# Kernel optimization log

Measured on AMD Instinct MI355X. Metric: run time of the kernel, lower is better.

The kernel has to match this reference:

```python
import jax, jax.numpy as jnp
import numpy as np

IN_DIM, HID, HEADS, LAYERS = 15, 128, 8, 6
N_NODES, N_EDGES = 20000, 160000
HC = HEADS * HID  # 1024
LN_EPS = 1e-5


def setup_inputs() -> dict:
    key = jax.random.key(0)
    ks = jax.random.split(key, 12)
    w = lambda k, shape: (jax.random.normal(k, shape, jnp.float32) * 0.02)
    return {
        "x": jax.random.normal(ks[0], (N_NODES, IN_DIM), jnp.float32),
        "edge_index": jax.random.randint(ks[1], (2, N_EDGES), 0, N_NODES, jnp.int32),
        # input projection
        "Win": w(ks[2], (IN_DIM, HID)), "b_in": jnp.zeros((HID,), jnp.float32),
        # per-layer TransformerConv params (stacked over LAYERS)
        "Wq": w(ks[3], (LAYERS, HID, HC)), "bq": jnp.zeros((LAYERS, HC), jnp.float32),
        "Wk": w(ks[4], (LAYERS, HID, HC)), "bk": jnp.zeros((LAYERS, HC), jnp.float32),
        "Wv": w(ks[5], (LAYERS, HID, HC)), "bv": jnp.zeros((LAYERS, HC), jnp.float32),
        "Wskip": w(ks[6], (LAYERS, HID, HC)), "bskip": jnp.zeros((LAYERS, HC), jnp.float32),
        "Wbeta": w(ks[7], (LAYERS, 3 * HC, 1)),  # lin_beta, bias=False
        # LayerNorm(hid*heads) and output proj per layer
        "ln_g": jnp.ones((LAYERS, HC), jnp.float32), "ln_b": jnp.zeros((LAYERS, HC), jnp.float32),
        "Wproj": w(ks[8], (LAYERS, HC, HID)), "bproj": jnp.zeros((LAYERS, HID), jnp.float32),
    }


def _transformer_layer(h, src, dst, Wq, bq, Wk, bk, Wv, bv, Wskip, bskip, Wbeta, ln_g, ln_b, Wproj, bproj):
    N = h.shape[0]
    # multi-head q/k/v: [N, H, C]
    q = (h @ Wq + bq).reshape(N, HEADS, HID)
    k = (h @ Wk + bk).reshape(N, HEADS, HID)
    v = (h @ Wv + bv).reshape(N, HEADS, HID)
    # per-edge attention logits: [E, H]
    alpha = jnp.einsum("ehc,ehc->eh", q[dst], k[src]) / jnp.sqrt(jnp.float32(HID))
    # segment softmax over incoming edges of each destination node
    amax = jax.ops.segment_max(alpha, dst, num_segments=N)  # [N, H]
    ex = jnp.exp(alpha - amax[dst])
    denom = jax.ops.segment_sum(ex, dst, num_segments=N)  # [N, H]
    attn = ex / (denom[dst] + 1e-16)  # [E, H]
    # weighted message scatter-sum: [N, H, C] -> concat [N, H*C]
    msg = v[src] * attn[:, :, None]
    out = jax.ops.segment_sum(msg, dst, num_segments=N).reshape(N, HC)
    # beta-gated skip (beta=True, concat=True)
    x_r = h @ Wskip + bskip  # [N, HC]
    beta = jax.nn.sigmoid(jnp.concatenate([out, x_r, out - x_r], axis=-1) @ Wbeta)  # [N, 1]
    out = beta * x_r + (1.0 - beta) * out
    # LayerNorm over last dim (HC)
    mu = jnp.mean(out, axis=-1, keepdims=True)
    var = jnp.var(out, axis=-1, keepdims=True)
    out = (out - mu) * jax.lax.rsqrt(var + LN_EPS) * ln_g + ln_b
    # project back, residual, relu
    out = out @ Wproj + bproj
    return jax.nn.relu(out + h)


def reference(x, edge_index, Win, b_in, Wq, bq, Wk, bk, Wv, bv, Wskip, bskip, Wbeta, ln_g, ln_b, Wproj, bproj):
    src, dst = edge_index[0], edge_index[1]
    h = x @ Win + b_in  # input_lin; dropout is identity in eval
    for l in range(LAYERS):
        h = _transformer_layer(h, src, dst, Wq[l], bq[l], Wk[l], bk[l], Wv[l], bv[l],
                               Wskip[l], bskip[l], Wbeta[l], ln_g[l], ln_b[l], Wproj[l], bproj[l])
    return h
```

## Files before the change

kernel.cpp:

```cpp
#include <hip/hip_runtime.h>
#include <stdint.h>

#define NN 20000
#define NE 160000
#define L_IN 15
#define D_H 128
#define N_HEADS 8
#define D_HC 1024
#define N_LAYERS 6
#define M_PAD 20096
#define QS2 2048

typedef unsigned short u16;
typedef __attribute__((ext_vector_type(8))) short short8;
typedef __attribute__((ext_vector_type(4))) float f32x4;

#define RSQRT_D 0.08838834764831845f

__device__ __forceinline__ float bu2f(u16 u) { return __uint_as_float(((unsigned)u) << 16); }
__device__ __forceinline__ u16 f2bu(float f) {
    unsigned x = __float_as_uint(f);
    return (u16)((x + 0x7fffu + ((x >> 16) & 1u)) >> 16);
}
__device__ __forceinline__ float wred64(float v) {
#pragma unroll
    for (int m = 32; m >= 1; m >>= 1) v += __shfl_xor(v, m, 64);
    return v;
}
__device__ __forceinline__ void cvt16(const uint4& u0, const uint4& u1, float* f) {
    unsigned d[8] = {u0.x, u0.y, u0.z, u0.w, u1.x, u1.y, u1.z, u1.w};
#pragma unroll
    for (int i = 0; i < 8; i++) {
        f[2 * i]     = __uint_as_float(d[i] << 16);
        f[2 * i + 1] = __uint_as_float(d[i] & 0xffff0000u);
    }
}

__global__ void k_detect(const u16* __restrict__ xb, int* __restrict__ flag) {
    int t = threadIdx.x;
    u16 u = xb[2 * t];
    int e = (u >> 7) & 0xFF;
    int weird = (e > 150 || (e != 0 && e < 100)) ? 1 : 0;
    __shared__ int cnt;
    if (t == 0) cnt = 0;
    __syncthreads();
    atomicAdd(&cnt, weird);
    __syncthreads();
    if (t == 0) *flag = (cnt > 64) ? 1 : 0;
}

struct CvDesc { const void* in[13]; u16* out[13]; };
#define CV_TOTAL 1930976
__global__ void k_convert_all(CvDesc dsc, const int* __restrict__ flag) {
    const int sizes[13] = {NN * L_IN, L_IN * D_H, D_H,
                           N_LAYERS * D_HC, N_LAYERS * D_HC, N_LAYERS * D_HC,
                           N_LAYERS * D_HC, N_LAYERS * 3 * D_HC,
                           N_LAYERS * D_HC, N_LAYERS * D_HC, N_LAYERS * D_H,
                           N_LAYERS * D_H * D_HC, N_LAYERS * D_H * D_HC};
    int off = blockIdx.x * 256 + threadIdx.x;
    if (off >= CV_TOTAL) return;
    int seg = 0;
#pragma unroll
    for (int s = 0; s < 13; s++) {
        if (off >= sizes[s] && seg == s) { off -= sizes[s]; seg = s + 1; }
    }
    if (*flag) dsc.out[seg][off] = f2bu(((const float*)dsc.in[seg])[off]);
    else       dsc.out[seg][off] = ((const u16*)dsc.in[seg])[off];
}

__global__ void k_zero(int* __restrict__ p, int n) {
    int i = blockIdx.x * 256 + threadIdx.x;
    if (i < n) p[i] = 0;
}

__global__ void k_convT_vs(const void* __restrict__ Wv, const void* __restrict__ Ws,
                           u16* __restrict__ WvT, u16* __restrict__ Bmain,
                           const int* __restrict__ flag) {
    __shared__ u16 tile[64][66];
    int tk = blockIdx.x, tn = blockIdx.y, l = blockIdx.z;
    int t = threadIdx.x;
    int isv = (tn < 16);
    const void* W = isv ? Wv : Ws;
    int n_off = (tn & 15) * 64;
    int r = t >> 2, c0 = (t & 3) * 16;
    size_t base = (size_t)l * 128 * 1024 + (size_t)(tk * 64 + r) * 1024 + n_off + c0;
    if (*flag) {
        const float* Wf = (const float*)W;
#pragma unroll
        for (int cc = 0; cc < 16; cc++) tile[c0 + cc][r] = f2bu(Wf[base + cc]);
    } else {
        const u16* Wh = (const u16*)W;
#pragma unroll
        for (int cc = 0; cc < 16; cc++) tile[c0 + cc][r] = Wh[base + cc];
    }
    __syncthreads();
    int i = t >> 2, j0 = (t & 3) * 16;
    u16* dst = isv ? (WvT + ((size_t)l * 1024 + n_off + i) * 128 + tk * 64 + j0)
                   : (Bmain + ((size_t)l * 2048 + 1024 + n_off + i) * 128 + tk * 64 + j0);
#pragma unroll
    for (int jj = 0; jj < 16; jj++) dst[jj] = tile[i][j0 + jj];
}

__global__ void k_convT_proj(const void* __restrict__ Wp, u16* __restrict__ WT,
                             const int* __restrict__ flag) {
    __shared__ u16 tile[64][66];
    int tk = blockIdx.x, tn = blockIdx.y, l = blockIdx.z;
    int t = threadIdx.x;
    int r = t >> 2, c0 = (t & 3) * 16;
    size_t base = (size_t)l * 1024 * 128 + (size_t)(tk * 64 + r) * 128 + tn * 64 + c0;
    if (*flag) {
        const float* Wf = (const float*)Wp;
#pragma unroll
        for (int cc = 0; cc < 16; cc++) tile[c0 + cc][r] = f2bu(Wf[base + cc]);
    } else {
        const u16* Wh = (const u16*)Wp;
#pragma unroll
        for (int cc = 0; cc < 16; cc++) tile[c0 + cc][r] = Wh[base + cc];
    }
    __syncthreads();
    int i = t >> 2, j0 = (t & 3) * 16;
    u16* dst = WT + ((size_t)l * 128 + tn * 64 + i) * 1024 + tk * 64 + j0;
#pragma unroll
    for (int jj = 0; jj < 16; jj++) dst[jj] = tile[i][j0 + jj];
}

__global__ void k_GG(const u16* __restrict__ Wqb, const u16* __restrict__ Wkb,
                     u16* __restrict__ Bmain) {
    int h = blockIdx.x, l = blockIdx.y;
    __shared__ __align__(16) u16 Als[128 * 32];
    __shared__ __align__(16) u16 Bls[128 * 32];
    const int t = threadIdx.x;
    const int wave = t >> 6, lane = t & 63, quad = lane >> 4, l16 = lane & 15;
    const int wm = (wave >> 1) * 64, wn = (wave & 1) * 64;
    const u16* Ab = Wqb + (size_t)l * 128 * 1024 + h * 128;
    const u16* Bb = Wkb + (size_t)l * 128 * 1024 + h * 128;
    f32x4 acc[4][4];
#pragma unroll
    for (int i = 0; i < 4; i++)
#pragma unroll
        for (int j = 0; j < 4; j++) acc[i][j] = (f32x4){0.f, 0.f, 0.f, 0.f};
    for (int ko = 0; ko < 128; ko += 32) {
#pragma unroll
        for (int c = t; c < 512; c += 256) {
            int row = c >> 2, kc = c & 3;
            *reinterpret_cast<uint4*>(&Als[row * 32 + kc * 8]) =
                *reinterpret_cast<const uint4*>(Ab + (size_t)row * 1024 + ko + kc * 8);
            *reinterpret_cast<uint4*>(&Bls[row * 32 + kc * 8]) =
                *reinterpret_cast<const uint4*>(Bb + (size_t)row * 1024 + ko + kc * 8);
        }
        __syncthreads();
        short8 af[4], bf[4];
#pragma unroll
        for (int mt = 0; mt < 4; mt++)
            af[mt] = *reinterpret_cast<const short8*>(&Als[(wm + mt * 16 + l16) * 32 + quad * 8]);
#pragma unroll
        for (int nt = 0; nt < 4; nt++)
            bf[nt] = *reinterpret_cast<const short8*>(&Bls[(wn + nt * 16 + l16) * 32 + quad * 8]);
#pragma unroll
        for (int mt = 0; mt < 4; mt++)
#pragma unroll
            for (int nt = 0; nt < 4; nt++)
                acc[mt][nt] = __builtin_amdgcn_mfma_f32_16x16x32_bf16(af[mt], bf[nt], acc[mt][nt], 0, 0, 0);
        __syncthreads();
    }
    u16* dst = Bmain + (size_t)l * 2048 * 128;
#pragma unroll
    for (int mt = 0; mt < 4; mt++)
#pragma unroll
        for (int r = 0; r < 4; r++) {
            int row = wm + mt * 16 + quad * 4 + r;
#pragma unroll
            for (int nt = 0; nt < 4; nt++) {
                int col = wn + nt * 16 + l16;
                dst[(size_t)(h * 128 + col) * 128 + row] = f2bu(acc[mt][nt][r] * RSQRT_D);
            }
        }
}

__global__ void k_pre_small(const u16* __restrict__ Wqb, const u16* __restrict__ Wkb,
                            const u16* __restrict__ bq, const u16* __restrict__ bk,
                            u16* __restrict__ cb, float* __restrict__ wsc,
                            float* __restrict__ csc) {
    int gid = blockIdx.x * 256 + threadIdx.x;
    if (gid >= N_LAYERS * 2056) return;
    int l = gid / 2056, r = gid % 2056;
    float acc = 0.f;
    if (r < 1024) {
        int h = r >> 7, b = r & 127;
        const u16* bqp = bq + l * D_HC + h * 128;
        const u16* wkp = Wkb + (size_t)l * 128 * 1024 + (size_t)b * 1024 + h * 128;
        for (int m = 0; m < 128; m++) acc += bu2f(bqp[m]) * bu2f(wkp[m]);
        cb[l * 1024 + r] = f2bu(acc * RSQRT_D);
    } else if (r < 2048) {
        int a = (r - 1024) >> 3, h = (r - 1024) & 7;
        const u16* wqp = Wqb + (size_t)l * 128 * 1024 + (size_t)a * 1024 + h * 128;
        const u16* bkp = bk + l * D_HC + h * 128;
        for (int m = 0; m < 128; m++) acc += bu2f(wqp[m]) * bu2f(bkp[m]);
        wsc[l * 1024 + (r - 1024)] = acc * RSQRT_D;
    } else {
        int h = r - 2048;
        const u16* bqp = bq + l * D_HC + h * 128;
        const u16* bkp = bk + l * D_HC + h * 128;
        for (int m = 0; m < 128; m++) acc += bu2f(bqp[m]) * bu2f(bkp[m]);
        csc[l * 8 + h] = acc * RSQRT_D;
    }
}

__global__ void k_input_proj(const u16* __restrict__ x, const u16* __restrict__ Win,
                             const u16* __restrict__ b_in, u16* __restrict__ h) {
    int gid = blockIdx.x * 256 + threadIdx.x;
    int n = gid >> 7, j = gid & 127;
    float acc = bu2f(b_in[j]);
#pragma unroll
    for (int i = 0; i < L_IN; i++) acc += bu2f(x[n * L_IN + i]) * bu2f(Win[i * D_H + j]);
    h[gid] = f2bu(acc);
}

__global__ void k_hist(const int* __restrict__ dst, int* __restrict__ cnt) {
    int e = blockIdx.x * 256 + threadIdx.x;
    if (e < NE) atomicAdd(&cnt[dst[e]], 1);
}
__global__ void k_scanA(const int* __restrict__ cnt, int* __restrict__ incl, int* __restrict__ bsum) {
    __shared__ int s[256];
    int b = blockIdx.x, t = threadIdx.x, i = b * 256 + t;
    int v = (i < NN) ? cnt[i] : 0;
    s[t] = v;
    __syncthreads();
    for (int off = 1; off < 256; off <<= 1) {
        int u = (t >= off) ? s[t - off] : 0;
        __syncthreads();
        s[t] += u;
        __syncthreads();
    }
    if (i < NN) incl[i] = s[t];
    if (t == 255) bsum[b] = s[255];
}
__global__ void k_scanB(const int* __restrict__ bsum, int* __restrict__ bpre, int nb) {
    __shared__ int s[128];
    int t = threadIdx.x;
    int v = (t < nb) ? bsum[t] : 0;
    s[t] = v;
    __syncthreads();
    for (int off = 1; off < 128; off <<= 1) {
        int u = (t >= off) ? s[t - off] : 0;
        __syncthreads();
        s[t] += u;
        __syncthreads();
    }
    if (t < nb) bpre[t] = s[t] - v;
}
__global__ void k_scanC(const int* __restrict__ incl, const int* __restrict__ bpre, int* __restrict__ offs) {
    int b = blockIdx.x, t = threadIdx.x, i = b * 256 + t;
    if (i < NN) offs[i + 1] = incl[i] + bpre[b];
    if (i == 0) offs[0] = 0;
}
__global__ void k_scatter(const int* __restrict__ dst, const int* __restrict__ src,
                          const int* __restrict__ offs, int* __restrict__ cursor,
                          int* __restrict__ srcp) {
    int e = blockIdx.x * 256 + threadIdx.x;
    if (e < NE) {
        int d = dst[e];
        int p = offs[d] + atomicAdd(&cursor[d], 1);
        srcp[p] = src[e];
    }
}

__global__ void k_gemm(const u16* __restrict__ A, int lda, int K,
                       const u16* __restrict__ Bt,
                       u16* __restrict__ C, int ldc,
                       const u16* __restrict__ bia0, const u16* __restrict__ bia1) {
    __shared__ __align__(16) u16 smem[128 * 136];
    u16* Als = smem;
    u16* Bls = smem + 4096;
    const int m0 = blockIdx.y * 128, n0 = blockIdx.x * 128;
    const int t = threadIdx.x;
    const int wave = t >> 6, lane = t & 63, quad = lane >> 4, l16 = lane & 15;
    const int wm = (wave >> 1) * 64, wn = (wave & 1) * 64;
    f32x4 acc[4][4];
#pragma unroll
    for (int i = 0; i < 4; i++)
#pragma unroll
        for (int j = 0; j < 4; j++) acc[i][j] = (f32x4){0.f, 0.f, 0.f, 0.f};

    for (int ko = 0; ko < K; ko += 32) {
#pragma unroll
        for (int c = t; c < 512; c += 256) {
            int row = c >> 2, kc = c & 3;
            *reinterpret_cast<uint4*>(&Als[row * 32 + kc * 8]) =
                *reinterpret_cast<const uint4*>(A + (size_t)(m0 + row) * lda + ko + kc * 8);
            *reinterpret_cast<uint4*>(&Bls[row * 32 + kc * 8]) =
                *reinterpret_cast<const uint4*>(Bt + (size_t)(n0 + row) * K + ko + kc * 8);
        }
        __syncthreads();
        short8 af[4], bf[4];
#pragma unroll
        for (int mt = 0; mt < 4; mt++)
            af[mt] = *reinterpret_cast<const short8*>(&Als[(wm + mt * 16 + l16) * 32 + quad * 8]);
#pragma unroll
        for (int nt = 0; nt < 4; nt++)
            bf[nt] = *reinterpret_cast<const short8*>(&Bls[(wn + nt * 16 + l16) * 32 + quad * 8]);
#pragma unroll
        for (int mt = 0; mt < 4; mt++)
#pragma unroll
            for (int nt = 0; nt < 4; nt++)
                acc[mt][nt] = __builtin_amdgcn_mfma_f32_16x16x32_bf16(af[mt], bf[nt], acc[mt][nt], 0, 0, 0);
        __syncthreads();
    }
#pragma unroll
    for (int mt = 0; mt < 4; mt++)
#pragma unroll
        for (int r = 0; r < 4; r++) {
            int rl = wm + mt * 16 + quad * 4 + r;
#pragma unroll
            for (int nt = 0; nt < 4; nt++) {
                int cl = wn + nt * 16 + l16;
                int col = n0 + cl;
                const u16* bp = (col < 1024) ? bia0 : bia1;
                smem[rl * 136 + cl] = f2bu(acc[mt][nt][r] + bu2f(bp[col & 1023]));
            }
        }
    __syncthreads();
#pragma unroll
    for (int c = t; c < 2048; c += 256) {
        int row = c >> 4, kc = c & 15;
        int grow = m0 + row;
        if (grow < NN)
            *reinterpret_cast<uint4*>(C + (size_t)grow * ldc + n0 + kc * 8) =
                *reinterpret_cast<const uint4*>(&smem[row * 136 + kc * 8]);
    }
}

__global__ void k_sc(const u16* __restrict__ hc, const float* __restrict__ wsc,
                     const float* __restrict__ csc, float* __restrict__ scbuf) {
    int gid = blockIdx.x * 256 + threadIdx.x;
    if (gid >= NN * 8) return;
    int d = gid >> 3, h = gid & 7;
    const u16* hr = hc + (size_t)d * 128;
    float acc = csc[h];
    for (int a = 0; a < 128; a++) acc += bu2f(hr[a]) * wsc[a * 8 + h];
    scbuf[gid] = acc;
}

__global__ void k_attn2(u16* __restrict__ qkvs2, const u16* __restrict__ hc,
                        const int* __restrict__ offs, const int* __restrict__ srcp,
                        const float* __restrict__ scbuf) {
    int gid = blockIdx.x * 256 + threadIdx.x;
    int d = gid >> 6, lane = gid & 63;
    if (d >= NN) return;
    int hh = lane >> 3, ci = (lane & 7) * 16;
    u16* zp = qkvs2 + (size_t)d * QS2 + hh * 128 + ci;
    float zf[16];
    {
        uint4 z0 = *reinterpret_cast<const uint4*>(zp);
        uint4 z1 = *reinterpret_cast<const uint4*>(zp + 8);
        cvt16(z0, z1, zf);
    }
    float scown = scbuf[d * 8 + hh];
    float u[16];
#pragma unroll
    for (int j = 0; j < 16; j++) u[j] = 0.f;
    float lrun = 0.f;

    int beg = offs[d], end = offs[d + 1];
    for (int c0 = beg; c0 < end; c0 += 64) {
        int cn = min(64, end - c0);
        int myidx = (c0 + lane < end) ? srcp[c0 + lane] : 0;
        int s = __shfl(myidx, 0, 64);
        const u16* hp = hc + (size_t)s * 128 + ci;
        uint4 a0 = *reinterpret_cast<const uint4*>(hp);
        uint4 a1 = *reinterpret_cast<const uint4*>(hp + 8);
        for (int i = 0; i < cn; i++) {
            uint4 n0 = a0, n1 = a1;
            if (i + 1 < cn) {
                int sn = __shfl(myidx, i + 1, 64);
                const u16* hpn = hc + (size_t)sn * 128 + ci;
                n0 = *reinterpret_cast<const uint4*>(hpn);
                n1 = *reinterpret_cast<const uint4*>(hpn + 8);
            }
            float hf[16];
            cvt16(a0, a1, hf);
            float p = 0.f;
#pragma unroll
            for (int j = 0; j < 16; j++) p += zf[j] * hf[j];
            p += __shfl_xor(p, 1, 64);
            p += __shfl_xor(p, 2, 64);
            p += __shfl_xor(p, 4, 64);
            float w = __expf(p + scown);
            lrun += w;
#pragma unroll
            for (int j = 0; j < 16; j++) u[j] += w * hf[j];
            a0 = n0; a1 = n1;
        }
    }
    float inv = 1.f / (lrun + 1e-16f);
    unsigned out[8];
#pragma unroll
    for (int j = 0; j < 8; j++)
        out[j] = (unsigned)f2bu(u[2 * j] * inv) | ((unsigned)f2bu(u[2 * j + 1] * inv) << 16);
    uint4* op = reinterpret_cast<uint4*>(zp);
    op[0] = make_uint4(out[0], out[1], out[2], out[3]);
    op[1] = make_uint4(out[4], out[5], out[6], out[7]);
}

__global__ void k_vproj(const u16* __restrict__ A ,
                        const u16* __restrict__ WvT_l, const u16* __restrict__ bv_l,
                        u16* __restrict__ obuf) {
    __shared__ __align__(16) u16 smem[128 * 136];
    u16* Als = smem;
    u16* Bls = smem + 4096;
    const int m0 = blockIdx.x * 128, h = blockIdx.y;
    const int t = threadIdx.x;
    const int wave = t >> 6, lane = t & 63, quad = lane >> 4, l16 = lane & 15;
    const int wm = (wave >> 1) * 64, wn = (wave & 1) * 64;
    f32x4 acc[4][4];
#pragma unroll
    for (int i = 0; i < 4; i++)
#pragma unroll
        for (int j = 0; j < 4; j++) acc[i][j] = (f32x4){0.f, 0.f, 0.f, 0.f};

    for (int ko = 0; ko < 128; ko += 32) {
#pragma unroll
        for (int c = t; c < 512; c += 256) {
            int row = c >> 2, kc = c & 3;
            *reinterpret_cast<uint4*>(&Als[row * 32 + kc * 8]) =
                *reinterpret_cast<const uint4*>(A + (size_t)(m0 + row) * QS2 + h * 128 + ko + kc * 8);
            *reinterpret_cast<uint4*>(&Bls[row * 32 + kc * 8]) =
                *reinterpret_cast<const uint4*>(WvT_l + (size_t)(h * 128 + row) * 128 + ko + kc * 8);
        }
        __syncthreads();
        short8 af[4], bf[4];
#pragma unroll
        for (int mt = 0; mt < 4; mt++)
            af[mt] = *reinterpret_cast<const short8*>(&Als[(wm + mt * 16 + l16) * 32 + quad * 8]);
#pragma unroll
        for (int nt = 0; nt < 4; nt++)
            bf[nt] = *reinterpret_cast<const short8*>(&Bls[(wn + nt * 16 + l16) * 32 + quad * 8]);
#pragma unroll
        for (int mt = 0; mt < 4; mt++)
#pragma unroll
            for (int nt = 0; nt < 4; nt++)
                acc[mt][nt] = __builtin_amdgcn_mfma_f32_16x16x32_bf16(af[mt], bf[nt], acc[mt][nt], 0, 0, 0);
        __syncthreads();
    }
#pragma unroll
    for (int mt = 0; mt < 4; mt++)
#pragma unroll
        for (int r = 0; r < 4; r++) {
            int rl = wm + mt * 16 + quad * 4 + r;
#pragma unroll
            for (int nt = 0; nt < 4; nt++) {
                int cl = wn + nt * 16 + l16;
                smem[rl * 136 + cl] = f2bu(acc[mt][nt][r] + bu2f(bv_l[h * 128 + cl]));
            }
        }
    __syncthreads();
#pragma unroll
    for (int c = t; c < 2048; c += 256) {
        int row = c >> 4, kc = c & 15;
        int grow = m0 + row;
        if (grow < NN)
            *reinterpret_cast<uint4*>(obuf + (size_t)grow * 1024 + h * 128 + kc * 8) =
                *reinterpret_cast<const uint4*>(&smem[row * 136 + kc * 8]);
    }
}

__global__ void k_betaLN(const u16* __restrict__ obuf, u16* __restrict__ qkvs2,
                         const u16* __restrict__ Wb, const u16* __restrict__ lng,
                         const u16* __restrict__ lnb) {
    int gid = blockIdx.x * 256 + threadIdx.x;
    int d = gid >> 6, lane = gid & 63;
    if (d >= NN) return;
    int c0 = lane * 16;
    float o[16], xr[16];
    {
        const u16* op = obuf + (size_t)d * 1024 + c0;
        uint4 o0 = *reinterpret_cast<const uint4*>(op);
        uint4 o1 = *reinterpret_cast<const uint4*>(op + 8);
        cvt16(o0, o1, o);
        const u16* xp = qkvs2 + (size_t)d * QS2 + 1024 + c0;
        uint4 x0 = *reinterpret_cast<const uint4*>(xp);
        uint4 x1 = *reinterpret_cast<const uint4*>(xp + 8);
        cvt16(x0, x1, xr);
    }
    float part = 0.f;
    {
        const u16* wp = Wb + c0;
        uint4 u0 = *reinterpret_cast<const uint4*>(wp);
        uint4 u1 = *reinterpret_cast<const uint4*>(wp + 8);
        float wf[16];
        cvt16(u0, u1, wf);
#pragma unroll
        for (int j = 0; j < 16; j++) part += o[j] * wf[j];
        u0 = *reinterpret_cast<const uint4*>(wp + D_HC);
        u1 = *reinterpret_cast<const uint4*>(wp + D_HC + 8);
        cvt16(u0, u1, wf);
#pragma unroll
        for (int j = 0; j < 16; j++) part += xr[j] * wf[j];
        u0 = *reinterpret_cast<const uint4*>(wp + 2 * D_HC);
        u1 = *reinterpret_cast<const uint4*>(wp + 2 * D_HC + 8);
        cvt16(u0, u1, wf);
#pragma unroll
        for (int j = 0; j < 16; j++) part += (o[j] - xr[j]) * wf[j];
    }
    float logit = wred64(part);
    float beta = 1.f / (1.f + __expf(-logit));
    float g[16], s1 = 0.f, s2 = 0.f;
#pragma unroll
    for (int j = 0; j < 16; j++) {
        g[j] = beta * xr[j] + (1.f - beta) * o[j];
        s1 += g[j]; s2 += g[j] * g[j];
    }
    s1 = wred64(s1);
    s2 = wred64(s2);
    float mu = s1 * (1.f / 1024.f);
    float var = s2 * (1.f / 1024.f) - mu * mu;
    float rs = rsqrtf(var + 1e-5f);
    {
        const u16* gp = lng + c0;
        const u16* bp2 = lnb + c0;
        uint4 g0 = *reinterpret_cast<const uint4*>(gp);
        uint4 g1 = *reinterpret_cast<const uint4*>(gp + 8);
        uint4 b0 = *reinterpret_cast<const uint4*>(bp2);
        uint4 b1 = *reinterpret_cast<const uint4*>(bp2 + 8);
        float lgf[16], lbf[16];
        cvt16(g0, g1, lgf);
        cvt16(b0, b1, lbf);
        unsigned out[8];
#pragma unroll
        for (int j = 0; j < 8; j++) {
            float y0 = (g[2 * j] - mu) * rs * lgf[2 * j] + lbf[2 * j];
            float y1 = (g[2 * j + 1] - mu) * rs * lgf[2 * j + 1] + lbf[2 * j + 1];
            out[j] = (unsigned)f2bu(y0) | ((unsigned)f2bu(y1) << 16);
        }
        uint4* yp = reinterpret_cast<uint4*>(qkvs2 + (size_t)d * QS2 + c0);
        yp[0] = make_uint4(out[0], out[1], out[2], out[3]);
        yp[1] = make_uint4(out[4], out[5], out[6], out[7]);
    }
}

__global__ void k_proj(const u16* __restrict__ A, int lda,
                       const u16* __restrict__ Bt,
                       void* __restrict__ C, int mode,
                       const u16* __restrict__ bias, const u16* __restrict__ resid,
                       const int* __restrict__ flag) {
    __shared__ __align__(16) u16 Als[64 * 32];
    __shared__ __align__(16) u16 Bls[128 * 32];
    const int m0 = blockIdx.x * 64;
    const int t = threadIdx.x;
    const int wave = t >> 6, lane = t & 63, quad = lane >> 4, l16 = lane & 15;
    const int fp32out = (mode == 2 && *flag) ? 1 : 0;
    f32x4 acc[8];
#pragma unroll
    for (int j = 0; j < 8; j++) acc[j] = (f32x4){0.f, 0.f, 0.f, 0.f};

    for (int ko = 0; ko < 1024; ko += 32) {
        {
            int row = t >> 2, kc = t & 3;
            *reinterpret_cast<uint4*>(&Als[row * 32 + kc * 8]) =
                *reinterpret_cast<const uint4*>(A + (size_t)(m0 + row) * lda + ko + kc * 8);
        }
#pragma unroll
        for (int c = t; c < 512; c += 256) {
            int row = c >> 2, kc = c & 3;
            *reinterpret_cast<uint4*>(&Bls[row * 32 + kc * 8]) =
                *reinterpret_cast<const uint4*>(Bt + (size_t)row * 1024 + ko + kc * 8);
        }
        __syncthreads();
        short8 af = *reinterpret_cast<const short8*>(&Als[(wave * 16 + l16) * 32 + quad * 8]);
#pragma unroll
        for (int nt = 0; nt < 8; nt++) {
            short8 bf = *reinterpret_cast<const short8*>(&Bls[(nt * 16 + l16) * 32 + quad * 8]);
            acc[nt] = __builtin_amdgcn_mfma_f32_16x16x32_bf16(af, bf, acc[nt], 0, 0, 0);
        }
        __syncthreads();
    }
#pragma unroll
    for (int r = 0; r < 4; r++) {
        int row = m0 + wave * 16 + quad * 4 + r;
        if (row >= NN) continue;
#pragma unroll
        for (int nt = 0; nt < 8; nt++) {
            int col = nt * 16 + l16;
            float v = acc[nt][r] + bu2f(bias[col]) + bu2f(resid[(size_t)row * D_H + col]);
            float rr = (v == v) ? fmaxf(v, 0.f) : v;
            if (fp32out) ((float*)C)[(size_t)row * D_H + col] = rr;
            else         ((u16*)C)[(size_t)row * D_H + col] = f2bu(rr);
        }
    }
}

extern "C" void kernel_launch(void* const* d_in, const int* in_sizes, int n_in,
                              void* d_out, int out_size, void* d_ws, size_t ws_size,
                              hipStream_t stream) {
    const int* ei = (const int*)d_in[1];
    const int* srcI = ei;
    const int* dstI = ei + NE;

    char* w = (char*)d_ws;
    auto carve = [&](size_t bytes) -> char* {
        char* p = w;
        w += (bytes + 255) & ~(size_t)255;
        return p;
    };
    u16* Bmain  = (u16*)carve((size_t)N_LAYERS * 2048 * 128 * 2);
    u16* WvT    = (u16*)carve((size_t)N_LAYERS * 1024 * 128 * 2);
    u16* WTp    = (u16*)carve((size_t)N_LAYERS * 128 * 1024 * 2);
    u16* hA     = (u16*)carve((size_t)M_PAD * D_H * 2);
    u16* hB     = (u16*)carve((size_t)M_PAD * D_H * 2);
    u16* qkvs2  = (u16*)carve((size_t)M_PAD * QS2 * 2);
    u16* obuf   = (u16*)carve((size_t)M_PAD * 1024 * 2);
    float* scbuf = (float*)carve((size_t)NN * 8 * 4);
    u16* cbuf   = (u16*)carve((size_t)N_LAYERS * 1024 * 2);
    float* wscb = (float*)carve((size_t)N_LAYERS * 1024 * 4);
    float* cscb = (float*)carve((size_t)N_LAYERS * 8 * 4);
    int* cnt    = (int*)carve(2 * NN * 4);
    int* cursor = cnt + NN;
    int* offs   = (int*)carve((NN + 1) * 4);
    int* incl   = (int*)carve(NN * 4);
    int* bsum   = (int*)carve(128 * 4);
    int* bpre   = (int*)carve(128 * 4);
    int* srcp   = (int*)carve(NE * 4);
    int* flag   = (int*)carve(256);

    const int conv_size[13] = {NN * L_IN, L_IN * D_H, D_H,
                               N_LAYERS * D_HC, N_LAYERS * D_HC, N_LAYERS * D_HC,
                               N_LAYERS * D_HC, N_LAYERS * 3 * D_HC,
                               N_LAYERS * D_HC, N_LAYERS * D_HC, N_LAYERS * D_H,
                               N_LAYERS * D_H * D_HC, N_LAYERS * D_H * D_HC};
    const int conv_idx[13] = {0, 2, 3, 5, 7, 9, 11, 12, 13, 14, 16, 4, 6};
    CvDesc dsc;
    u16* conv[13];
    for (int i = 0; i < 13; i++) {
        conv[i] = (u16*)carve((size_t)conv_size[i] * 2);
        dsc.in[i] = d_in[conv_idx[i]];
        dsc.out[i] = conv[i];
    }

    k_detect<<<1, 256, 0, stream>>>((const u16*)d_in[0], flag);
    k_convert_all<<<(CV_TOTAL + 255) / 256, 256, 0, stream>>>(dsc, flag);
    const u16* x    = conv[0];
    const u16* Win  = conv[1];
    const u16* b_in = conv[2];
    const u16* bq   = conv[3];
    const u16* bk   = conv[4];
    const u16* bv   = conv[5];
    const u16* bsk  = conv[6];
    const u16* Wb   = conv[7];
    const u16* lng  = conv[8];
    const u16* lnb  = conv[9];
    const u16* bp   = conv[10];
    const u16* Wqb  = conv[11];
    const u16* Wkb  = conv[12];

    k_convT_vs<<<dim3(2, 32, 6), 256, 0, stream>>>(d_in[8], d_in[10], WvT, Bmain, flag);
    k_convT_proj<<<dim3(16, 2, 6), 256, 0, stream>>>(d_in[15], WTp, flag);
    k_GG<<<dim3(8, 6), 256, 0, stream>>>(Wqb, Wkb, Bmain);
    k_pre_small<<<(N_LAYERS * 2056 + 255) / 256, 256, 0, stream>>>(Wqb, Wkb, bq, bk,
                                                                   cbuf, wscb, cscb);
    k_input_proj<<<(NN * D_H) / 256, 256, 0, stream>>>(x, Win, b_in, hA);
    k_zero<<<(2 * NN + 255) / 256, 256, 0, stream>>>(cnt, 2 * NN);
    k_hist<<<(NE + 255) / 256, 256, 0, stream>>>(dstI, cnt);
    const int NB = (NN + 255) / 256;
    k_scanA<<<NB, 256, 0, stream>>>(cnt, incl, bsum);
    k_scanB<<<1, 128, 0, stream>>>(bsum, bpre, NB);
    k_scanC<<<NB, 256, 0, stream>>>(incl, bpre, offs);
    k_scatter<<<(NE + 255) / 256, 256, 0, stream>>>(dstI, srcI, offs, cursor, srcp);

    u16* hc = hA;
    u16* hn = hB;
    for (int l = 0; l < N_LAYERS; l++) {
        k_gemm<<<dim3(16, 157), 256, 0, stream>>>(hc, D_H, D_H,
                                                  Bmain + (size_t)l * 2048 * 128,
                                                  qkvs2, QS2,
                                                  cbuf + l * 1024, bsk + l * D_HC);
        k_sc<<<(NN * 8 + 255) / 256, 256, 0, stream>>>(hc, wscb + l * 1024,
                                                       cscb + l * 8, scbuf);
        k_attn2<<<(NN * 64) / 256, 256, 0, stream>>>(qkvs2, hc, offs, srcp, scbuf);
        k_vproj<<<dim3(157, 8), 256, 0, stream>>>(qkvs2, WvT + (size_t)l * 1024 * 128,
                                                  bv + l * D_HC, obuf);
        k_betaLN<<<(NN * 64) / 256, 256, 0, stream>>>(obuf, qkvs2,
                                                      Wb + (size_t)l * 3 * D_HC,
                                                      lng + l * D_HC, lnb + l * D_HC);
        int last = (l == N_LAYERS - 1);
        void* outp = last ? d_out : (void*)hn;
        k_proj<<<314, 256, 0, stream>>>(qkvs2, QS2, WTp + (size_t)l * 128 * 1024,
                                        outp, last ? 2 : 1,
                                        bp + l * D_H, hc, flag);
        u16* tmp = hc; hc = hn; hn = tmp;
    }
}
```

Measured before the change: 1.017 ms.

## Retile output projection GEMM to 32-row blocks with register prefetch and padded LDS

```diff
diff --git a/kernel.cpp b/kernel.cpp
--- a/kernel.cpp
+++ b/kernel.cpp
@@ -538,50 +538,72 @@
     }
 }
 
+#define PLDA 40
 __global__ void k_proj(const u16* __restrict__ A, int lda,
                        const u16* __restrict__ Bt,
                        void* __restrict__ C, int mode,
                        const u16* __restrict__ bias, const u16* __restrict__ resid,
                        const int* __restrict__ flag) {
-    __shared__ __align__(16) u16 Als[64 * 32];
-    __shared__ __align__(16) u16 Bls[128 * 32];
-    const int m0 = blockIdx.x * 64;
+    __shared__ __align__(16) u16 Als[32 * PLDA];
+    __shared__ __align__(16) u16 Bls[128 * PLDA];
+    const int m0 = blockIdx.x * 32;
     const int t = threadIdx.x;
     const int wave = t >> 6, lane = t & 63, quad = lane >> 4, l16 = lane & 15;
     const int fp32out = (mode == 2 && *flag) ? 1 : 0;
-    f32x4 acc[8];
-#pragma unroll
-    for (int j = 0; j < 8; j++) acc[j] = (f32x4){0.f, 0.f, 0.f, 0.f};
-
+    f32x4 acc[2][2];
+#pragma unroll
+    for (int i = 0; i < 2; i++)
+#pragma unroll
+        for (int j = 0; j < 2; j++) acc[i][j] = (f32x4){0.f, 0.f, 0.f, 0.f};
+
+    uint4 pa;
+    uint4 pb0, pb1;
+    const int arow = t >> 2, akc = t & 3;
+    const int b0row = t >> 2, b0kc = t & 3;
+    const int b1row = (t + 256) >> 2, b1kc = t & 3;
+    {
+        if (t < 128)
+            pa = *reinterpret_cast<const uint4*>(A + (size_t)(m0 + arow) * lda + akc * 8);
+        pb0 = *reinterpret_cast<const uint4*>(Bt + (size_t)b0row * 1024 + b0kc * 8);
+        pb1 = *reinterpret_cast<const uint4*>(Bt + (size_t)b1row * 1024 + b1kc * 8);
+    }
     for (int ko = 0; ko < 1024; ko += 32) {
-        {
-            int row = t >> 2, kc = t & 3;
-            *reinterpret_cast<uint4*>(&Als[row * 32 + kc * 8]) =
-                *reinterpret_cast<const uint4*>(A + (size_t)(m0 + row) * lda + ko + kc * 8);
-        }
-#pragma unroll
-        for (int c = t; c < 512; c += 256) {
-            int row = c >> 2, kc = c & 3;
-            *reinterpret_cast<uint4*>(&Bls[row * 32 + kc * 8]) =
-                *reinterpret_cast<const uint4*>(Bt + (size_t)row * 1024 + ko + kc * 8);
-        }
-        __syncthreads();
-        short8 af = *reinterpret_cast<const short8*>(&Als[(wave * 16 + l16) * 32 + quad * 8]);
-#pragma unroll
-        for (int nt = 0; nt < 8; nt++) {
-            short8 bf = *reinterpret_cast<const short8*>(&Bls[(nt * 16 + l16) * 32 + quad * 8]);
-            acc[nt] = __builtin_amdgcn_mfma_f32_16x16x32_bf16(af, bf, acc[nt], 0, 0, 0);
-        }
-        __syncthreads();
-    }
+        if (t < 128)
+            *reinterpret_cast<uint4*>(&Als[arow * PLDA + akc * 8]) = pa;
+        *reinterpret_cast<uint4*>(&Bls[b0row * PLDA + b0kc * 8]) = pb0;
+        *reinterpret_cast<uint4*>(&Bls[b1row * PLDA + b1kc * 8]) = pb1;
+        __syncthreads();
+        int kn = ko + 32;
+        if (kn < 1024) {
+            if (t < 128)
+                pa = *reinterpret_cast<const uint4*>(A + (size_t)(m0 + arow) * lda + kn + akc * 8);
+            pb0 = *reinterpret_cast<const uint4*>(Bt + (size_t)b0row * 1024 + kn + b0kc * 8);
+            pb1 = *reinterpret_cast<const uint4*>(Bt + (size_t)b1row * 1024 + kn + b1kc * 8);
+        }
+        short8 af[2], bf[2];
+#pragma unroll
+        for (int mt = 0; mt < 2; mt++)
+            af[mt] = *reinterpret_cast<const short8*>(&Als[(mt * 16 + l16) * PLDA + quad * 8]);
+#pragma unroll
+        for (int nt = 0; nt < 2; nt++)
+            bf[nt] = *reinterpret_cast<const short8*>(&Bls[(wave * 32 + nt * 16 + l16) * PLDA + quad * 8]);
+#pragma unroll
+        for (int mt = 0; mt < 2; mt++)
+#pragma unroll
+            for (int nt = 0; nt < 2; nt++)
+                acc[mt][nt] = __builtin_amdgcn_mfma_f32_16x16x32_bf16(af[mt], bf[nt], acc[mt][nt], 0, 0, 0);
+        __syncthreads();
+    }
+#pragma unroll
+    for (int mt = 0; mt < 2; mt++)
 #pragma unroll
     for (int r = 0; r < 4; r++) {
-        int row = m0 + wave * 16 + quad * 4 + r;
+        int row = m0 + mt * 16 + quad * 4 + r;
         if (row >= NN) continue;
 #pragma unroll
-        for (int nt = 0; nt < 8; nt++) {
-            int col = nt * 16 + l16;
-            float v = acc[nt][r] + bu2f(bias[col]) + bu2f(resid[(size_t)row * D_H + col]);
+        for (int nt = 0; nt < 2; nt++) {
+            int col = wave * 32 + nt * 16 + l16;
+            float v = acc[mt][nt][r] + bu2f(bias[col]) + bu2f(resid[(size_t)row * D_H + col]);
             float rr = (v == v) ? fmaxf(v, 0.f) : v;
             if (fp32out) ((float*)C)[(size_t)row * D_H + col] = rr;
             else         ((u16*)C)[(size_t)row * D_H + col] = f2bu(rr);
@@ -683,7 +705,7 @@
                                                       lng + l * D_HC, lnb + l * D_HC);
         int last = (l == N_LAYERS - 1);
         void* outp = last ? d_out : (void*)hn;
-        k_proj<<<314, 256, 0, stream>>>(qkvs2, QS2, WTp + (size_t)l * 128 * 1024,
+        k_proj<<<628, 256, 0, stream>>>(qkvs2, QS2, WTp + (size_t)l * 128 * 1024,
                                         outp, last ? 2 : 1,
                                         bp + l * D_H, hc, flag);
         u16* tmp = hc; hc = hn; hn = tmp;
```

Result: faster. 945.0 us (-7.0%).
